# Performance work log

Hardware: AMD Instinct MI355X
Metric: run time of the kernel (lower is better)

## Reference

```python
import jax, jax.numpy as jnp
import numpy as np

NUM_HEADS = 16


def setup_inputs() -> dict:
    key = jax.random.key(0)
    ks = jax.random.split(key, 5)
    B, S, H = 2, 2048, 1024
    scale = 0.02
    return {
        "x": jax.random.normal(ks[0], (B, S, H), dtype=jnp.float32),
        "w_qkv": jax.random.normal(ks[1], (H, 3 * H), dtype=jnp.float32) * scale,
        "b_qkv": jax.random.normal(ks[2], (3 * H,), dtype=jnp.float32) * scale,
        "w_out": jax.random.normal(ks[3], (H, H), dtype=jnp.float32) * scale,
        "b_out": jax.random.normal(ks[4], (H,), dtype=jnp.float32) * scale,
    }


def reference(x, w_qkv, b_qkv, w_out, b_out):
    B, S, H = x.shape
    nh = NUM_HEADS
    hd = H // nh
    attn_scale = 1.0 / np.sqrt(hd).astype(np.float32)

    qkv = x @ w_qkv + b_qkv                       # (B, S, 3H)
    q, k, v = jnp.split(qkv, 3, axis=-1)
    # (B, S, H) -> (B, nh, S, hd)
    to_heads = lambda t: t.reshape(B, S, nh, hd).transpose(0, 2, 1, 3)
    q, k, v = to_heads(q), to_heads(k), to_heads(v)

    scores = jnp.einsum("bhid,bhjd->bhij", q, k) * attn_scale  # (B, nh, S, S)
    # Source masks where triu(ones)==0 -> strictly-lower triangle masked;
    # allowed positions are j >= i (attends to present and future).
    i = jnp.arange(S)[:, None]
    j = jnp.arange(S)[None, :]
    scores = jnp.where(j >= i, scores, -jnp.inf)
    attn = jax.nn.softmax(scores, axis=-1)        # dropout is identity (eval)

    out = jnp.einsum("bhij,bhjd->bhid", attn, v)  # (B, nh, S, hd)
    out = out.transpose(0, 2, 1, 3).reshape(B, S, H)
    return out @ w_out + b_out
```

## Files before the change

kernel.cpp:

```cpp
#include <hip/hip_runtime.h>
#include <hip/hip_bf16.h>
#include <stdint.h>
#include <stddef.h>

typedef __bf16 bf16_t;
typedef __bf16 bf16x4 __attribute__((ext_vector_type(4)));
typedef __bf16 bf16x8 __attribute__((ext_vector_type(8)));
typedef float f32x4 __attribute__((ext_vector_type(4)));
typedef float f32x16 __attribute__((ext_vector_type(16)));

#define MFMA16(a, b, c) __builtin_amdgcn_mfma_f32_16x16x32_bf16(a, b, c, 0, 0, 0)
#define MFMA32(a, b, c) __builtin_amdgcn_mfma_f32_32x32x16_bf16(a, b, c, 0, 0, 0)

#define GLL16(g, l)                                                      \
    __builtin_amdgcn_global_load_lds(                                    \
        (const __attribute__((address_space(1))) void*)(g),              \
        (__attribute__((address_space(3))) void*)(l), 16, 0, 0)

#define SEQ 2048
#define NHEAD 16
#define HD 64
#define HID 1024
#define QKV_LD 3072
#define VT_LD 2080

__global__ __launch_bounds__(256)
void prep_kernel(const float* __restrict__ x, const float* __restrict__ w_qkv,
                 const float* __restrict__ w_out, bf16_t* __restrict__ xbf,
                 bf16_t* __restrict__ wqkvT, bf16_t* __restrict__ woutT) {
    int L = blockIdx.x;
    int tid = threadIdx.x;
    if (L < 4096) {
        int i = (L * 256 + tid) * 4;
        float4 v = *(const float4*)(x + i);
        bf16x4 o = {(bf16_t)v.x, (bf16_t)v.y, (bf16_t)v.z, (bf16_t)v.w};
        *(bf16x4*)(xbf + i) = o;
        return;
    }
    __shared__ bf16_t tile[32][33];
    const float* W;
    bf16_t* Wt;
    int N, bx, by;
    if (L < 7168) {
        int r = L - 4096;
        W = w_qkv; Wt = wqkvT; N = 3072; bx = r % 96; by = r / 96;
    } else {
        int r = L - 7168;
        W = w_out; Wt = woutT; N = 1024; bx = r % 32; by = r / 32;
    }
    int K = 1024;
    int n0 = bx * 32, k0 = by * 32;
    int tx = tid & 31, ty = tid >> 5;
#pragma unroll
    for (int i = 0; i < 4; i++)
        tile[ty + i * 8][tx] = (bf16_t)W[(size_t)(k0 + ty + i * 8) * N + n0 + tx];
    __syncthreads();
#pragma unroll
    for (int i = 0; i < 4; i++)
        Wt[(size_t)(n0 + ty + i * 8) * K + k0 + tx] = tile[tx][ty + i * 8];
}

#define STAGE8(GB, LB, KOFF)                                                   \
    do {                                                                       \
        GLL16((GB) + (size_t)srow * K + (KOFF) + ssw,                          \
              (LB) + srow * 64 + (scl << 3));                                  \
        GLL16((GB) + (size_t)(srow + 64) * K + (KOFF) + ssw,                   \
              (LB) + (srow + 64) * 64 + (scl << 3));                           \
    } while (0)

__global__ __launch_bounds__(512, 2)
void gemm_qkv_8ph(const bf16_t* __restrict__ A, const bf16_t* __restrict__ Bt,
                  const float* __restrict__ bias, bf16_t* __restrict__ C,
                  bf16_t* __restrict__ Vt, int M, int N, int K) {
    __shared__ __align__(16) bf16_t As[2][256][64];
    __shared__ __align__(16) bf16_t Bs[2][256][64];

    int nbx = N >> 8;
    int bid = blockIdx.x;
    int swz = (bid & 7) * (gridDim.x >> 3) + (bid >> 3);
    int m0 = (swz / nbx) << 8;
    int n0 = (swz % nbx) << 8;

    int tid = threadIdx.x;
    int lane = tid & 63;
    int wave = tid >> 6;
    int l16 = lane & 15, quad = lane >> 4;
    int wm = (wave >> 2) << 7;
    int wn = (wave & 3) << 6;

    int srow = tid >> 3;
    int scl = tid & 7;
    int ssw = ((scl ^ (srow & 7)) << 3);

    const bf16_t* Ab = A + (size_t)m0 * K;
    const bf16_t* Bb = Bt + (size_t)n0 * K;

    f32x4 acc[8][4] = {};
    bf16x8 af[4][2], b0[2][2], b1[2][2];

    const int NT = K >> 6;

    STAGE8(Bb, &Bs[0][0][0], 0);
    STAGE8(Ab, &As[0][0][0], 0);
    STAGE8(Bb + (size_t)128 * K, &Bs[0][128][0], 0);
    STAGE8(Ab + (size_t)128 * K, &As[0][128][0], 0);
    STAGE8(Bb, &Bs[1][0][0], 64);
    STAGE8(Ab, &As[1][0][0], 64);
    asm volatile("s_waitcnt vmcnt(4)" ::: "memory");
    __builtin_amdgcn_s_barrier();

    for (int t = 0; t < NT; t++) {
        int buf = t & 1;
        const bf16_t* Asb = &As[buf][0][0];
        const bf16_t* Bsb = &Bs[buf][0][0];
        int k1 = (t + 1) << 6;
        int k2 = (t + 2) << 6;

#pragma unroll
        for (int mt = 0; mt < 4; mt++) {
            int row = wm + mt * 16 + l16;
#pragma unroll
            for (int ks = 0; ks < 2; ks++)
                af[mt][ks] = *(const bf16x8*)(
                    Asb + row * 64 + (((ks * 4 + quad) ^ (row & 7)) << 3));
        }
#pragma unroll
        for (int nt = 0; nt < 2; nt++) {
            int row = wn + nt * 16 + l16;
#pragma unroll
            for (int ks = 0; ks < 2; ks++)
                b0[nt][ks] = *(const bf16x8*)(
                    Bsb + row * 64 + (((ks * 4 + quad) ^ (row & 7)) << 3));
        }
        if (t + 1 < NT) STAGE8(Bb + (size_t)128 * K, &Bs[buf ^ 1][128][0], k1);
        __builtin_amdgcn_s_barrier();
        asm volatile("s_waitcnt lgkmcnt(0)" ::: "memory");
        __builtin_amdgcn_s_setprio(1);
#pragma unroll
        for (int mt = 0; mt < 4; mt++)
#pragma unroll
            for (int nt = 0; nt < 2; nt++)
#pragma unroll
                for (int ks = 0; ks < 2; ks++)
                    acc[mt][nt] = MFMA16(af[mt][ks], b0[nt][ks], acc[mt][nt]);
        __builtin_amdgcn_s_setprio(0);
        __builtin_amdgcn_s_barrier();

#pragma unroll
        for (int nt = 0; nt < 2; nt++) {
            int row = wn + 32 + nt * 16 + l16;
#pragma unroll
            for (int ks = 0; ks < 2; ks++)
                b1[nt][ks] = *(const bf16x8*)(
                    Bsb + row * 64 + (((ks * 4 + quad) ^ (row & 7)) << 3));
        }
        if (t + 1 < NT) STAGE8(Ab + (size_t)128 * K, &As[buf ^ 1][128][0], k1);
        __builtin_amdgcn_s_barrier();
        asm volatile("s_waitcnt lgkmcnt(0)" ::: "memory");
        __builtin_amdgcn_s_setprio(1);
#pragma unroll
        for (int mt = 0; mt < 4; mt++)
#pragma unroll
            for (int nt = 0; nt < 2; nt++)
#pragma unroll
                for (int ks = 0; ks < 2; ks++)
                    acc[mt][2 + nt] =
                        MFMA16(af[mt][ks], b1[nt][ks], acc[mt][2 + nt]);
        __builtin_amdgcn_s_setprio(0);
        __builtin_amdgcn_s_barrier();

#pragma unroll
        for (int mt = 0; mt < 4; mt++) {
            int row = wm + 64 + mt * 16 + l16;
#pragma unroll
            for (int ks = 0; ks < 2; ks++)
                af[mt][ks] = *(const bf16x8*)(
                    Asb + row * 64 + (((ks * 4 + quad) ^ (row & 7)) << 3));
        }
        if (t + 2 < NT) STAGE8(Bb, &Bs[buf][0][0], k2);
        __builtin_amdgcn_s_barrier();
        asm volatile("s_waitcnt lgkmcnt(0)" ::: "memory");
        __builtin_amdgcn_s_setprio(1);
#pragma unroll
        for (int mt = 0; mt < 4; mt++)
#pragma unroll
            for (int nt = 0; nt < 2; nt++)
#pragma unroll
                for (int ks = 0; ks < 2; ks++)
                    acc[4 + mt][nt] =
                        MFMA16(af[mt][ks], b0[nt][ks], acc[4 + mt][nt]);
        __builtin_amdgcn_s_setprio(0);
        __builtin_amdgcn_s_barrier();

        if (t + 2 < NT) {
            STAGE8(Ab, &As[buf][0][0], k2);
            asm volatile("s_waitcnt vmcnt(4)" ::: "memory");
        } else if (t + 1 < NT) {
            asm volatile("s_waitcnt vmcnt(0)" ::: "memory");
        }
        __builtin_amdgcn_s_barrier();
        __builtin_amdgcn_s_setprio(1);
#pragma unroll
        for (int mt = 0; mt < 4; mt++)
#pragma unroll
            for (int nt = 0; nt < 2; nt++)
#pragma unroll
                for (int ks = 0; ks < 2; ks++)
                    acc[4 + mt][2 + nt] =
                        MFMA16(af[mt][ks], b1[nt][ks], acc[4 + mt][2 + nt]);
        __builtin_amdgcn_s_setprio(0);
        __builtin_amdgcn_s_barrier();
    }

    if (n0 < 2048) {
#pragma unroll
        for (int mi = 0; mi < 8; mi++) {
            int row = m0 + wm + (mi >> 2) * 64 + (mi & 3) * 16 + quad * 4;
#pragma unroll
            for (int ni = 0; ni < 4; ni++) {
                int col = n0 + wn + (ni >> 1) * 32 + (ni & 1) * 16 + l16;
                float bv = bias[col];
#pragma unroll
                for (int r = 0; r < 4; r++)
                    C[(size_t)(row + r) * N + col] = (bf16_t)(acc[mi][ni][r] + bv);
            }
        }
    } else {
#pragma unroll
        for (int mi = 0; mi < 8; mi++) {
            int row = m0 + wm + (mi >> 2) * 64 + (mi & 3) * 16 + quad * 4;
            int b = row >> 11, s = row & 2047;
#pragma unroll
            for (int ni = 0; ni < 4; ni++) {
                int col = n0 + wn + (ni >> 1) * 32 + (ni & 1) * 16 + l16;
                float bv = bias[col];
                int cv = col - 2048;
                int bh = b * 16 + (cv >> 6);
                bf16x4 pk;
#pragma unroll
                for (int r = 0; r < 4; r++)
                    pk[r] = (bf16_t)(acc[mi][ni][r] + bv);
                *(bf16x4*)(Vt + ((size_t)bh * HD + (cv & 63)) * VT_LD + s) = pk;
            }
        }
    }
}

template <typename OutT, int TN>
__global__ __launch_bounds__(256)
void gemm_bt_bias(const bf16_t* __restrict__ A, const bf16_t* __restrict__ Bt,
                  const float* __restrict__ bias, OutT* __restrict__ C,
                  int M, int N, int K) {
    constexpr int NT = TN / 32;
    __shared__ __align__(16) bf16_t As[128][32];
    __shared__ __align__(16) bf16_t Bs[TN][32];

    int m0 = blockIdx.y * 128;
    int n0 = blockIdx.x * TN;
    int tid = threadIdx.x;
    int wave = tid >> 6, lane = tid & 63;
    int quad = lane >> 4, l16 = lane & 15;
    int wm = (wave >> 1) * 64, wn = (wave & 1) * (TN / 2);

    f32x4 acc[4][NT] = {};

    const bf16_t* a_base =
        A + (size_t)(m0 + wave * 32 + (lane >> 2)) * K + (lane & 3) * 8;
    const bf16_t* b_base =
        Bt + (size_t)(n0 + wave * (TN / 4) + (lane >> 2)) * K + (lane & 3) * 8;
    bf16_t* as_base = &As[wave * 32][0];
    bf16_t* bs_base = &Bs[wave * (TN / 4)][0];

    for (int k0 = 0; k0 < K; k0 += 32) {
        GLL16(a_base + k0, as_base);
        GLL16(a_base + 16 * K + k0, as_base + 16 * 32);
        GLL16(b_base + k0, bs_base);
        if (TN == 128) GLL16(b_base + 16 * K + k0, bs_base + 16 * 32);
        __syncthreads();

        bf16x8 af[4], bfr[NT];
#pragma unroll
        for (int t = 0; t < 4; t++)
            af[t] = *(const bf16x8*)(&As[wm + t * 16 + l16][quad * 8]);
#pragma unroll
        for (int t = 0; t < NT; t++)
            bfr[t] = *(const bf16x8*)(&Bs[wn + t * 16 + l16][quad * 8]);
#pragma unroll
        for (int mt = 0; mt < 4; mt++)
#pragma unroll
            for (int nt = 0; nt < NT; nt++)
                acc[mt][nt] = MFMA16(af[mt], bfr[nt], acc[mt][nt]);
        __syncthreads();
    }

#pragma unroll
    for (int mt = 0; mt < 4; mt++) {
        int row = m0 + wm + mt * 16 + quad * 4;
#pragma unroll
        for (int nt = 0; nt < NT; nt++) {
            int col = n0 + wn + nt * 16 + l16;
            float bv = bias[col];
#pragma unroll
            for (int r = 0; r < 4; r++)
                C[(size_t)(row + r) * N + col] = (OutT)(acc[mt][nt][r] + bv);
        }
    }
}

__global__ __launch_bounds__(512, 4)
void attn_kernel(const bf16_t* __restrict__ qkv, const bf16_t* __restrict__ Vt,
                 bf16_t* __restrict__ attn_out) {
    int bh = blockIdx.x;
    int tile = (blockIdx.y < 8) ? blockIdx.y : (23 - blockIdx.y);
    int b = bh >> 4, h = bh & 15;

    int tid = threadIdx.x, wave = tid >> 6, lane = tid & 63;
    int l32 = lane & 31, hi = lane >> 5;
    int ih = wave >> 1, jh = wave & 1;

    const bf16_t* q_g = qkv + (size_t)b * SEQ * QKV_LD + (size_t)h * HD;
    const bf16_t* k_g = q_g + HID;
    const bf16_t* vt_g = Vt + (size_t)bh * HD * VT_LD;

    __shared__ __align__(16) bf16_t Ks[64][72];
    __shared__ __align__(16) bf16_t Vs[64][72];
    __shared__ __align__(16) bf16_t Ps[128][68];
    __shared__ float lsumS[8][32];

    const float QS = 0.125f * 1.44269504088896f;
    int i0 = tile * 128;

    bf16x8 qa[4];
    {
        const bf16_t* qrow = q_g + (size_t)(i0 + ih * 32 + l32) * QKV_LD + hi * 8;
#pragma unroll
        for (int ks = 0; ks < 4; ks++) {
            bf16x8 t = *(const bf16x8*)(qrow + ks * 16);
#pragma unroll
            for (int e = 0; e < 8; e++) qa[ks][e] = (bf16_t)((float)t[e] * QS);
        }
    }

    f32x16 o = {};
    float lsum = 0.0f;

    int sr = tid >> 3, sc = (tid & 7) * 8;

    bf16x8 kr = *(const bf16x8*)(k_g + (size_t)(i0 + sr) * QKV_LD + sc);
    bf16x8 vr = *(const bf16x8*)(vt_g + (size_t)sr * VT_LD + i0 + sc);

    for (int j0 = i0; j0 < SEQ; j0 += 64) {
        __syncthreads();
        *(bf16x8*)(&Ks[sr][sc]) = kr;
        *(bf16x8*)(&Vs[sr][sc]) = vr;
        __syncthreads();

        if (j0 + 64 < SEQ) {
            kr = *(const bf16x8*)(k_g + (size_t)(j0 + 64 + sr) * QKV_LD + sc);
            vr = *(const bf16x8*)(vt_g + (size_t)sr * VT_LD + j0 + 64 + sc);
        }

        f32x16 st = {};
#pragma unroll
        for (int ks = 0; ks < 4; ks++) {
            bf16x8 ka = *(const bf16x8*)(&Ks[jh * 32 + l32][ks * 16 + hi * 8]);
            st = MFMA32(ka, qa[ks], st);
        }

        if (j0 < i0 + 128) {
            int gi = i0 + ih * 32 + l32;
#pragma unroll
            for (int rq = 0; rq < 4; rq++) {
                bf16x4 pk;
#pragma unroll
                for (int r = 0; r < 4; r++) {
                    int gj = j0 + jh * 32 + 8 * rq + 4 * hi + r;
                    float p = (gj >= gi) ? __builtin_amdgcn_exp2f(st[rq * 4 + r]) : 0.0f;
                    lsum += p;
                    pk[r] = (bf16_t)p;
                }
                *(bf16x4*)(&Ps[ih * 32 + l32][jh * 32 + 8 * rq + 4 * hi]) = pk;
            }
        } else {
#pragma unroll
            for (int rq = 0; rq < 4; rq++) {
                bf16x4 pk;
#pragma unroll
                for (int r = 0; r < 4; r++) {
                    float p = __builtin_amdgcn_exp2f(st[rq * 4 + r]);
                    lsum += p;
                    pk[r] = (bf16_t)p;
                }
                *(bf16x4*)(&Ps[ih * 32 + l32][jh * 32 + 8 * rq + 4 * hi]) = pk;
            }
        }
        __syncthreads();

#pragma unroll
        for (int ks = 0; ks < 4; ks++) {
            bf16x8 pa = *(const bf16x8*)(&Ps[ih * 32 + l32][ks * 16 + hi * 8]);
            bf16x8 vb = *(const bf16x8*)(&Vs[jh * 32 + l32][ks * 16 + hi * 8]);
            o = MFMA32(pa, vb, o);
        }
    }

    lsum += __shfl_xor(lsum, 32, 64);
    lsumS[wave][l32] = lsum;
    __syncthreads();

#pragma unroll
    for (int rq = 0; rq < 4; rq++) {
#pragma unroll
        for (int r = 0; r < 4; r++) {
            int il = 8 * rq + 4 * hi + r;
            float rs = lsumS[ih * 2][il] + lsumS[ih * 2 + 1][il];
            int gi = i0 + ih * 32 + il;
            attn_out[(size_t)(b * SEQ + gi) * HID + h * HD + jh * 32 + l32] =
                (bf16_t)(o[rq * 4 + r] / rs);
        }
    }
}

extern "C" void kernel_launch(void* const* d_in, const int* in_sizes, int n_in,
                              void* d_out, int out_size, void* d_ws, size_t ws_size,
                              hipStream_t stream) {
    const float* x     = (const float*)d_in[0];
    const float* w_qkv = (const float*)d_in[1];
    const float* b_qkv = (const float*)d_in[2];
    const float* w_out = (const float*)d_in[3];
    const float* b_out = (const float*)d_in[4];
    float* out = (float*)d_out;

    char* ws = (char*)d_ws;
    bf16_t* xbf   = (bf16_t*)(ws);
    bf16_t* wqkvT = (bf16_t*)(ws + 8388608);
    bf16_t* woutT = (bf16_t*)(ws + 14680064);
    bf16_t* qkv   = (bf16_t*)(ws + 16777216);
    bf16_t* attn  = (bf16_t*)(ws + 41943040);
    bf16_t* Vt    = (bf16_t*)(ws + 50331648);

    prep_kernel<<<8192, 256, 0, stream>>>(x, w_qkv, w_out, xbf, wqkvT, woutT);

    gemm_qkv_8ph<<<192, 512, 0, stream>>>(xbf, wqkvT, b_qkv, qkv, Vt,
                                          4096, 3072, 1024);

    attn_kernel<<<dim3(2 * NHEAD, SEQ / 128), 512, 0, stream>>>(qkv, Vt, attn);

    gemm_bt_bias<float, 64><<<dim3(1024 / 64, 4096 / 128), 256, 0, stream>>>(
        attn, woutT, b_out, out, 4096, 1024, 1024);
}
```

Baseline: 172.8 us.

## Restructure GEMM main loop to single-barrier double-buffer with full-tile prefetch

Replaces the interleaved, eight-barrier-per-iteration staging schedule with a simpler double buffer: all four global-to-LDS stages for the next K tile are issued at the top of the iteration, followed by one vmcnt wait and one barrier at the end. Per-step workgroup barriers are replaced with sched_barrier fences and partial lgkmcnt waits so that LDS fragment loads overlap the first MFMA block. The aim is to cut barrier overhead. The trade-off is a shallower prefetch (one tile ahead instead of staggered two-tile staging), which may expose more global memory latency.

New measurement: 178.3 us. 1.03x slower.

```diff
diff --git a/kernel.cpp b/kernel.cpp
--- a/kernel.cpp
+++ b/kernel.cpp
@@ -16,6 +16,8 @@
     __builtin_amdgcn_global_load_lds(                                    \
         (const __attribute__((address_space(1))) void*)(g),              \
         (__attribute__((address_space(3))) void*)(l), 16, 0, 0)
+
+#define SB0() __builtin_amdgcn_sched_barrier(0)
 
 #define SEQ 2048
 #define NHEAD 16
@@ -96,7 +98,7 @@
     const bf16_t* Bb = Bt + (size_t)n0 * K;
 
     f32x4 acc[8][4] = {};
-    bf16x8 af[4][2], b0[2][2], b1[2][2];
+    bf16x8 a[4][2], b0[2][2], b1[2][2];
 
     const int NT = K >> 6;
 
@@ -104,9 +106,7 @@
     STAGE8(Ab, &As[0][0][0], 0);
     STAGE8(Bb + (size_t)128 * K, &Bs[0][128][0], 0);
     STAGE8(Ab + (size_t)128 * K, &As[0][128][0], 0);
-    STAGE8(Bb, &Bs[1][0][0], 64);
-    STAGE8(Ab, &As[1][0][0], 64);
-    asm volatile("s_waitcnt vmcnt(4)" ::: "memory");
+    asm volatile("s_waitcnt vmcnt(0)" ::: "memory");
     __builtin_amdgcn_s_barrier();
 
     for (int t = 0; t < NT; t++) {
@@ -114,16 +114,25 @@
         const bf16_t* Asb = &As[buf][0][0];
         const bf16_t* Bsb = &Bs[buf][0][0];
         int k1 = (t + 1) << 6;
-        int k2 = (t + 2) << 6;
+
+        if (t + 1 < NT) {
+            bf16_t* Asn = &As[buf ^ 1][0][0];
+            bf16_t* Bsn = &Bs[buf ^ 1][0][0];
+            STAGE8(Bb, Bsn, k1);
+            STAGE8(Ab, Asn, k1);
+            STAGE8(Bb + (size_t)128 * K, Bsn + 128 * 64, k1);
+            STAGE8(Ab + (size_t)128 * K, Asn + 128 * 64, k1);
+        }
 
 #pragma unroll
         for (int mt = 0; mt < 4; mt++) {
             int row = wm + mt * 16 + l16;
 #pragma unroll
             for (int ks = 0; ks < 2; ks++)
-                af[mt][ks] = *(const bf16x8*)(
+                a[mt][ks] = *(const bf16x8*)(
                     Asb + row * 64 + (((ks * 4 + quad) ^ (row & 7)) << 3));
         }
+        SB0();
 #pragma unroll
         for (int nt = 0; nt < 2; nt++) {
             int row = wn + nt * 16 + l16;
@@ -132,20 +141,7 @@
                 b0[nt][ks] = *(const bf16x8*)(
                     Bsb + row * 64 + (((ks * 4 + quad) ^ (row & 7)) << 3));
         }
-        if (t + 1 < NT) STAGE8(Bb + (size_t)128 * K, &Bs[buf ^ 1][128][0], k1);
-        __builtin_amdgcn_s_barrier();
-        asm volatile("s_waitcnt lgkmcnt(0)" ::: "memory");
-        __builtin_amdgcn_s_setprio(1);
-#pragma unroll
-        for (int mt = 0; mt < 4; mt++)
-#pragma unroll
-            for (int nt = 0; nt < 2; nt++)
-#pragma unroll
-                for (int ks = 0; ks < 2; ks++)
-                    acc[mt][nt] = MFMA16(af[mt][ks], b0[nt][ks], acc[mt][nt]);
-        __builtin_amdgcn_s_setprio(0);
-        __builtin_amdgcn_s_barrier();
-
+        SB0();
 #pragma unroll
         for (int nt = 0; nt < 2; nt++) {
             int row = wn + 32 + nt * 16 + l16;
@@ -154,9 +150,23 @@
                 b1[nt][ks] = *(const bf16x8*)(
                     Bsb + row * 64 + (((ks * 4 + quad) ^ (row & 7)) << 3));
         }
-        if (t + 1 < NT) STAGE8(Ab + (size_t)128 * K, &As[buf ^ 1][128][0], k1);
-        __builtin_amdgcn_s_barrier();
+        SB0();
+
+        asm volatile("s_waitcnt lgkmcnt(4)" ::: "memory");
+        SB0();
+        __builtin_amdgcn_s_setprio(1);
+#pragma unroll
+        for (int mt = 0; mt < 4; mt++)
+#pragma unroll
+            for (int nt = 0; nt < 2; nt++)
+#pragma unroll
+                for (int ks = 0; ks < 2; ks++)
+                    acc[mt][nt] = MFMA16(a[mt][ks], b0[nt][ks], acc[mt][nt]);
+        __builtin_amdgcn_s_setprio(0);
+        SB0();
+
         asm volatile("s_waitcnt lgkmcnt(0)" ::: "memory");
+        SB0();
         __builtin_amdgcn_s_setprio(1);
 #pragma unroll
         for (int mt = 0; mt < 4; mt++)
@@ -165,21 +175,22 @@
 #pragma unroll
                 for (int ks = 0; ks < 2; ks++)
                     acc[mt][2 + nt] =
-                        MFMA16(af[mt][ks], b1[nt][ks], acc[mt][2 + nt]);
+                        MFMA16(a[mt][ks], b1[nt][ks], acc[mt][2 + nt]);
         __builtin_amdgcn_s_setprio(0);
-        __builtin_amdgcn_s_barrier();
+        SB0();
 
 #pragma unroll
         for (int mt = 0; mt < 4; mt++) {
             int row = wm + 64 + mt * 16 + l16;
 #pragma unroll
             for (int ks = 0; ks < 2; ks++)
-                af[mt][ks] = *(const bf16x8*)(
+                a[mt][ks] = *(const bf16x8*)(
                     Asb + row * 64 + (((ks * 4 + quad) ^ (row & 7)) << 3));
         }
-        if (t + 2 < NT) STAGE8(Bb, &Bs[buf][0][0], k2);
-        __builtin_amdgcn_s_barrier();
+        SB0();
+
         asm volatile("s_waitcnt lgkmcnt(0)" ::: "memory");
+        SB0();
         __builtin_amdgcn_s_setprio(1);
 #pragma unroll
         for (int mt = 0; mt < 4; mt++)
@@ -188,18 +199,7 @@
 #pragma unroll
                 for (int ks = 0; ks < 2; ks++)
                     acc[4 + mt][nt] =
-                        MFMA16(af[mt][ks], b0[nt][ks], acc[4 + mt][nt]);
-        __builtin_amdgcn_s_setprio(0);
-        __builtin_amdgcn_s_barrier();
-
-        if (t + 2 < NT) {
-            STAGE8(Ab, &As[buf][0][0], k2);
-            asm volatile("s_waitcnt vmcnt(4)" ::: "memory");
-        } else if (t + 1 < NT) {
-            asm volatile("s_waitcnt vmcnt(0)" ::: "memory");
-        }
-        __builtin_amdgcn_s_barrier();
-        __builtin_amdgcn_s_setprio(1);
+                        MFMA16(a[mt][ks], b0[nt][ks], acc[4 + mt][nt]);
 #pragma unroll
         for (int mt = 0; mt < 4; mt++)
 #pragma unroll
@@ -207,8 +207,11 @@
 #pragma unroll
                 for (int ks = 0; ks < 2; ks++)
                     acc[4 + mt][2 + nt] =
-                        MFMA16(af[mt][ks], b1[nt][ks], acc[4 + mt][2 + nt]);
+                        MFMA16(a[mt][ks], b1[nt][ks], acc[4 + mt][2 + nt]);
         __builtin_amdgcn_s_setprio(0);
+        SB0();
+
+        if (t + 1 < NT) asm volatile("s_waitcnt vmcnt(0)" ::: "memory");
         __builtin_amdgcn_s_barrier();
     }
 
```
